# Kernel tuning notes

Hardware: AMD Instinct MI355X
Metric: run time of the kernel (lower is better)

## Reference

```python
import jax, jax.numpy as jnp
import numpy as np

N_EMBD = 1024
HEAD_SIZE = 64
B, T = 8, 2048


def setup_inputs() -> dict:
    key = jax.random.key(0)
    k1, k2, k3, k4 = jax.random.split(key, 4)
    scale = 1.0 / np.sqrt(N_EMBD)
    return {
        "x": jax.random.normal(k1, (B, T, N_EMBD), dtype=jnp.float32),
        "Wq": jax.random.normal(k2, (N_EMBD, HEAD_SIZE), dtype=jnp.float32) * scale,
        "Wk": jax.random.normal(k3, (N_EMBD, HEAD_SIZE), dtype=jnp.float32) * scale,
        "Wv": jax.random.normal(k4, (N_EMBD, HEAD_SIZE), dtype=jnp.float32) * scale,
    }


def reference(x, Wq, Wk, Wv):
    # x: [B, T, C]; projections (no bias)
    q = jnp.einsum("btc,ch->bth", x, Wq)
    k = jnp.einsum("btc,ch->bth", x, Wk)
    v = jnp.einsum("btc,ch->bth", x, Wv)
    head_size = k.shape[-1]
    # scaled scores [B, T, T]
    wei = jnp.einsum("bth,bsh->bts", q, k) * (head_size ** -0.5)
    # causal mask (lower-triangular keeps)
    Tlen = x.shape[1]
    causal = jnp.tril(jnp.ones((Tlen, Tlen), dtype=bool))
    wei = jnp.where(causal[None, :, :], wei, -jnp.inf)
    wei = jax.nn.softmax(wei, axis=-1)
    # dropout p=0 (eval) -> identity
    out = jnp.einsum("bts,bsh->bth", wei, v)
    return out
```

## Files before the change

### kernel.cpp

```cpp
#include <hip/hip_runtime.h>
#include <hip/hip_bf16.h>
#include <math.h>

#define Bn 8
#define Tn 2048
#define Cn 1024
#define Hn 64

typedef __attribute__((ext_vector_type(8))) short short8;
typedef __attribute__((ext_vector_type(4))) float floatx4;

#define ATTN_SCALE 0.18033688011112042f

__device__ inline unsigned short f2bf(float f) {
    union { float f; unsigned int u; } x; x.f = f;
    unsigned int r = x.u + 0x7fffu + ((x.u >> 16) & 1u);
    return (unsigned short)(r >> 16);
}

__device__ inline uint2 pack4bf(float4 v) {
    __hip_bfloat162 lo = __float22bfloat162_rn(make_float2(v.x, v.y));
    __hip_bfloat162 hi = __float22bfloat162_rn(make_float2(v.z, v.w));
    uint2 r;
    r.x = *reinterpret_cast<unsigned int*>(&lo);
    r.y = *reinterpret_cast<unsigned int*>(&hi);
    return r;
}

__device__ inline float rsum16(float v) {
    v += __shfl_xor(v, 1);
    v += __shfl_xor(v, 2);
    v += __shfl_xor(v, 4);
    v += __shfl_xor(v, 8);
    return v;
}

__global__ __launch_bounds__(256) void prep_w(
    const float* __restrict__ Wq, const float* __restrict__ Wk,
    const float* __restrict__ Wv, unsigned short* __restrict__ Wfrag)
{
    const int gid = blockIdx.x * 256 + threadIdx.x;
    const int c    = gid >> 11;
    const int rem  = gid & 2047;
    const int ks   = rem >> 6;
    const int lane = rem & 63;
    const int ln = lane & 15, qd = lane >> 4;
    const int mat = c >> 2, nc = c & 3;
    const float* W = (mat == 0) ? Wq : (mat == 1) ? Wk : Wv;
    const float sc = (mat == 0) ? ATTN_SCALE : 1.0f;
    const int col = nc * 16 + ln;
    unsigned short o[8];
    #pragma unroll
    for (int j = 0; j < 8; ++j)
        o[j] = f2bf(W[(size_t)(ks * 32 + qd * 8 + j) * Hn + col] * sc);
    *reinterpret_cast<short8*>(Wfrag + (size_t)gid * 8) = *reinterpret_cast<short8*>(o);
}

__global__ __launch_bounds__(256, 4) void proj_mfma(
    const float* __restrict__ x, const unsigned short* __restrict__ Wfrag,
    unsigned short* __restrict__ qbf, unsigned short* __restrict__ kfrag,
    unsigned short* __restrict__ vfrag)
{
    __shared__ unsigned short xs[2][16][136];

    const int ln   = threadIdx.x & 15;
    const int quad = (threadIdx.x >> 4) & 3;
    const int w    = threadIdx.x >> 6;
    const int lane = threadIdx.x & 63;
    const int row0 = blockIdx.x * 16;

    const int srow = threadIdx.x >> 4;
    const int sf   = threadIdx.x & 15;
    const float4* xrow4 = reinterpret_cast<const float4*>(x + (size_t)(row0 + srow) * Cn);

    floatx4 acc[3];
    #pragma unroll
    for (int i = 0; i < 3; ++i) acc[i] = (floatx4){0.f, 0.f, 0.f, 0.f};

    float4 pa_ = xrow4[sf], pb_ = xrow4[sf + 16];
    *reinterpret_cast<uint2*>(&xs[0][srow][sf * 4])      = pack4bf(pa_);
    *reinterpret_cast<uint2*>(&xs[0][srow][sf * 4 + 64]) = pack4bf(pb_);
    pa_ = xrow4[32 + sf]; pb_ = xrow4[32 + sf + 16];

    for (int c = 0; c < 8; ++c) {
        __syncthreads();
        if (c < 7) {
            *reinterpret_cast<uint2*>(&xs[(c + 1) & 1][srow][sf * 4])      = pack4bf(pa_);
            *reinterpret_cast<uint2*>(&xs[(c + 1) & 1][srow][sf * 4 + 64]) = pack4bf(pb_);
        }
        if (c < 6) {
            pa_ = xrow4[(c + 2) * 32 + sf];
            pb_ = xrow4[(c + 2) * 32 + sf + 16];
        }
        #pragma unroll
        for (int kk = 0; kk < 4; ++kk) {
            const short8 a = *reinterpret_cast<const short8*>(
                &xs[c & 1][ln][kk * 32 + quad * 8]);
            #pragma unroll
            for (int i = 0; i < 3; ++i) {
                const int cc = w * 3 + i;
                const short8 b = *reinterpret_cast<const short8*>(
                    Wfrag + ((size_t)((cc * 32) + c * 4 + kk) * 64 + lane) * 8);
                acc[i] = __builtin_amdgcn_mfma_f32_16x16x32_bf16(a, b, acc[i], 0, 0, 0);
            }
        }
    }

    const int t0   = row0 + quad * 4;
    const int b    = t0 >> 11;
    const int tloc = t0 & 2047;
    #pragma unroll
    for (int i = 0; i < 3; ++i) {
        const int idx = w * 3 + i;
        const int mat = idx >> 2, ch = idx & 3;
        if (mat == 0) {
            #pragma unroll
            for (int r = 0; r < 4; ++r)
                qbf[(size_t)(t0 + r) * Hn + ch * 16 + ln] = f2bf(acc[i][r]);
        } else if (mat == 1) {
            const int kc = tloc >> 4;
            const int ks = ch >> 1;
            const int lq = (ch & 1) * 2 + (ln >> 3);
            #pragma unroll
            for (int r = 0; r < 4; ++r) {
                const int lanep = (quad * 4 + r) + 16 * lq;
                kfrag[(((size_t)(b * 128 + kc) * 2 + ks) * 64 + lanep) * 8 + (ln & 7)]
                    = f2bf(acc[i][r]);
            }
        } else {
            const int kb32 = tloc >> 5;
            const int off  = t0 & 31;
            const int qd   = off >> 3;
            const int j0   = off & 7;
            const int lanep = ln + 16 * qd;
            ushort4 pk;
            pk.x = f2bf(acc[i][0]); pk.y = f2bf(acc[i][1]);
            pk.z = f2bf(acc[i][2]); pk.w = f2bf(acc[i][3]);
            *reinterpret_cast<ushort4*>(
                vfrag + (((size_t)(b * 64 + kb32) * 4 + ch) * 64 + lanep) * 8 + j0) = pk;
        }
    }
}

__global__ __launch_bounds__(256) void attn_mfma(
    const unsigned short* __restrict__ qbf, const unsigned short* __restrict__ kfrag,
    const unsigned short* __restrict__ vfrag, float* __restrict__ out)
{
    __shared__ unsigned short p_lds[4][2][16 * 32];
    __shared__ float o_lds[4][32][68];
    __shared__ float l_lds[4][32];

    const int j  = blockIdx.x;
    const int b  = j & 7;
    const int ti = 63 - (j >> 3);
    const int q0 = ti * 32;

    const int ln   = threadIdx.x & 15;
    const int quad = (threadIdx.x >> 4) & 3;
    const int w    = threadIdx.x >> 6;
    const int lane = threadIdx.x & 63;

    const unsigned short* qb = qbf + (size_t)b * Tn * Hn;
    const unsigned short* Kb = kfrag + (size_t)b * 131072;
    const unsigned short* Vb = vfrag + (size_t)b * 131072;

    short8 aq[2][2];
    #pragma unroll
    for (int m = 0; m < 2; ++m)
        #pragma unroll
        for (int h = 0; h < 2; ++h)
            aq[m][h] = *reinterpret_cast<const short8*>(
                qb + (size_t)(q0 + m * 16 + ln) * Hn + h * 32 + quad * 8);

    floatx4 O[2][4];
    #pragma unroll
    for (int m = 0; m < 2; ++m)
        #pragma unroll
        for (int c = 0; c < 4; ++c) O[m][c] = (floatx4){0.f, 0.f, 0.f, 0.f};
    float lp[2][4] = {{0.f,0.f,0.f,0.f},{0.f,0.f,0.f,0.f}};

    const int ntiles = (q0 >> 5) + 1;
    const int per    = (ntiles + 3) >> 2;
    const int beg    = w * per;
    const int end    = min(beg + per, ntiles);

    short8 kf[4], vf[4];
    if (beg < end) {
        #pragma unroll
        for (int u = 0; u < 4; ++u) {
            kf[u] = *reinterpret_cast<const short8*>(Kb + ((size_t)(beg * 4 + u)) * 512 + lane * 8);
            vf[u] = *reinterpret_cast<const short8*>(Vb + ((size_t)(beg * 4 + u)) * 512 + lane * 8);
        }
    }

    for (int t = beg; t < end; ++t) {
        short8 kn[4], vn[4];
        const bool more = (t + 1) < end;
        if (more) {
            #pragma unroll
            for (int u = 0; u < 4; ++u) {
                kn[u] = *reinterpret_cast<const short8*>(Kb + ((size_t)((t + 1) * 4 + u)) * 512 + lane * 8);
                vn[u] = *reinterpret_cast<const short8*>(Vb + ((size_t)((t + 1) * 4 + u)) * 512 + lane * 8);
            }
        }
        const floatx4 z = (floatx4){0.f, 0.f, 0.f, 0.f};
        floatx4 S[2][2];
        #pragma unroll
        for (int m = 0; m < 2; ++m)
            #pragma unroll
            for (int s = 0; s < 2; ++s) {
                S[m][s] = __builtin_amdgcn_mfma_f32_16x16x32_bf16(aq[m][0], kf[s * 2], z, 0, 0, 0);
                S[m][s] = __builtin_amdgcn_mfma_f32_16x16x32_bf16(aq[m][1], kf[s * 2 + 1], S[m][s], 0, 0, 0);
            }
        const bool diag = (t == ntiles - 1);
        #pragma unroll
        for (int m = 0; m < 2; ++m) {
            #pragma unroll
            for (int s = 0; s < 2; ++s) {
                #pragma unroll
                for (int r = 0; r < 4; ++r) {
                    float sv = S[m][s][r];
                    if (diag && (s * 16 + ln > m * 16 + quad * 4 + r)) sv = -1e30f;
                    const float p = exp2f(sv);
                    lp[m][r] += p;
                    p_lds[w][m][(quad * 4 + r) * 32 + s * 16 + ln] = f2bf(p);
                }
            }
        }
        __asm__ volatile("s_waitcnt lgkmcnt(0)" ::: "memory");
        short8 pa[2];
        #pragma unroll
        for (int m = 0; m < 2; ++m)
            pa[m] = *reinterpret_cast<const short8*>(&p_lds[w][m][ln * 32 + quad * 8]);
        #pragma unroll
        for (int m = 0; m < 2; ++m)
            #pragma unroll
            for (int c = 0; c < 4; ++c)
                O[m][c] = __builtin_amdgcn_mfma_f32_16x16x32_bf16(pa[m], vf[c], O[m][c], 0, 0, 0);
        #pragma unroll
        for (int u = 0; u < 4; ++u) { kf[u] = kn[u]; vf[u] = vn[u]; }
    }

    #pragma unroll
    for (int m = 0; m < 2; ++m) {
        #pragma unroll
        for (int c = 0; c < 4; ++c)
            #pragma unroll
            for (int r = 0; r < 4; ++r)
                o_lds[w][m * 16 + quad * 4 + r][c * 16 + ln] = O[m][c][r];
        #pragma unroll
        for (int r = 0; r < 4; ++r) {
            const float ls = rsum16(lp[m][r]);
            if (ln == 0) l_lds[w][m * 16 + quad * 4 + r] = ls;
        }
    }
    __syncthreads();

    const int qq  = threadIdx.x >> 3;
    const int dgp = threadIdx.x & 7;
    const float ltot = l_lds[0][qq] + l_lds[1][qq] + l_lds[2][qq] + l_lds[3][qq];
    const float inv = 1.0f / ltot;
    float* op = out + ((size_t)b * Tn + q0 + qq) * Hn + dgp * 8;
    #pragma unroll
    for (int u = 0; u < 2; ++u) {
        const float4 a0 = *reinterpret_cast<float4*>(&o_lds[0][qq][dgp * 8 + u * 4]);
        const float4 a1 = *reinterpret_cast<float4*>(&o_lds[1][qq][dgp * 8 + u * 4]);
        const float4 a2 = *reinterpret_cast<float4*>(&o_lds[2][qq][dgp * 8 + u * 4]);
        const float4 a3 = *reinterpret_cast<float4*>(&o_lds[3][qq][dgp * 8 + u * 4]);
        float4 r;
        r.x = (a0.x + a1.x + a2.x + a3.x) * inv;
        r.y = (a0.y + a1.y + a2.y + a3.y) * inv;
        r.z = (a0.z + a1.z + a2.z + a3.z) * inv;
        r.w = (a0.w + a1.w + a2.w + a3.w) * inv;
        *reinterpret_cast<float4*>(op + u * 4) = r;
    }
}

extern "C" void kernel_launch(void* const* d_in, const int* in_sizes, int n_in,
                              void* d_out, int out_size, void* d_ws, size_t ws_size,
                              hipStream_t stream) {
    (void)in_sizes; (void)n_in; (void)out_size; (void)ws_size;
    const float* x  = (const float*)d_in[0];
    const float* Wq = (const float*)d_in[1];
    const float* Wk = (const float*)d_in[2];
    const float* Wv = (const float*)d_in[3];
    float* out = (float*)d_out;

    unsigned short* Wfrag = (unsigned short*)d_ws;
    unsigned short* qbf   = Wfrag + (size_t)196608;
    unsigned short* kfr   = qbf + (size_t)Bn * Tn * Hn;
    unsigned short* vfr   = kfr + (size_t)Bn * 131072;

    prep_w<<<96, 256, 0, stream>>>(Wq, Wk, Wv, Wfrag);
    proj_mfma<<<(Bn * Tn) / 16, 256, 0, stream>>>(x, Wfrag, qbf, kfr, vfr);
    attn_mfma<<<Bn * (Tn / 32), 256, 0, stream>>>(qbf, kfr, vfr, out);
}
```

Baseline: 133.7 us.

## Halve attention query tile to 16 rows, doubling blocks and raising occupancy

The attention kernel now handles 16 query rows per block instead of 32, so the grid is twice as large. Launch bounds ask for 4 blocks per CU, and the LDS buffers shrink, with the P tile row stride padded to 40 to reduce bank conflicts. V is loaded within the current iteration instead of being prefetched a tile ahead. The bf16 conversion of P now truncates instead of rounding, and the row sum uses the same truncated value. Each K/V tile is reused by half as many queries, so global and L2 traffic roughly doubles, traded for more parallelism and better load balance over the causal triangle.

```diff
diff --git a/kernel.cpp b/kernel.cpp
--- a/kernel.cpp
+++ b/kernel.cpp
@@ -142,18 +142,18 @@
     }
 }
 
-__global__ __launch_bounds__(256) void attn_mfma(
+__global__ __launch_bounds__(256, 4) void attn_mfma(
     const unsigned short* __restrict__ qbf, const unsigned short* __restrict__ kfrag,
-    const unsigned short* __restrict__ vfrag, float* __restrict__ out)
+    const unsigned short* __restrict__ vt, float* __restrict__ out)
 {
-    __shared__ unsigned short p_lds[4][2][16 * 32];
-    __shared__ float o_lds[4][32][68];
-    __shared__ float l_lds[4][32];
+    __shared__ unsigned short p_lds[4][16 * 40];
+    __shared__ float o_lds[4][16][68];
+    __shared__ float l_lds[4][16];
 
     const int j  = blockIdx.x;
     const int b  = j & 7;
-    const int ti = 63 - (j >> 3);
-    const int q0 = ti * 32;
+    const int ti = 127 - (j >> 3);
+    const int q0 = ti * 16;
 
     const int ln   = threadIdx.x & 15;
     const int quad = (threadIdx.x >> 4) & 3;
@@ -162,118 +162,93 @@
 
     const unsigned short* qb = qbf + (size_t)b * Tn * Hn;
     const unsigned short* Kb = kfrag + (size_t)b * 131072;
-    const unsigned short* Vb = vfrag + (size_t)b * 131072;
-
-    short8 aq[2][2];
-    #pragma unroll
-    for (int m = 0; m < 2; ++m)
-        #pragma unroll
-        for (int h = 0; h < 2; ++h)
-            aq[m][h] = *reinterpret_cast<const short8*>(
-                qb + (size_t)(q0 + m * 16 + ln) * Hn + h * 32 + quad * 8);
-
-    floatx4 O[2][4];
-    #pragma unroll
-    for (int m = 0; m < 2; ++m)
-        #pragma unroll
-        for (int c = 0; c < 4; ++c) O[m][c] = (floatx4){0.f, 0.f, 0.f, 0.f};
-    float lp[2][4] = {{0.f,0.f,0.f,0.f},{0.f,0.f,0.f,0.f}};
-
-    const int ntiles = (q0 >> 5) + 1;
+    const unsigned short* Vb = vt + (size_t)b * 131072;
+
+    const short8 aq0 = *reinterpret_cast<const short8*>(qb + (size_t)(q0 + ln) * Hn + quad * 8);
+    const short8 aq1 = *reinterpret_cast<const short8*>(qb + (size_t)(q0 + ln) * Hn + 32 + quad * 8);
+
+    floatx4 O[4];
+    #pragma unroll
+    for (int c = 0; c < 4; ++c) O[c] = (floatx4){0.f, 0.f, 0.f, 0.f};
+    float lp[4] = {0.f, 0.f, 0.f, 0.f};
+
+    const int ntiles = (q0 + 47) >> 5;
     const int per    = (ntiles + 3) >> 2;
     const int beg    = w * per;
     const int end    = min(beg + per, ntiles);
-
-    short8 kf[4], vf[4];
+    unsigned short* pP = p_lds[w];
+
+    short8 kf[4];
     if (beg < end) {
         #pragma unroll
+        for (int u = 0; u < 4; ++u)
+            kf[u] = *reinterpret_cast<const short8*>(Kb + ((size_t)(beg * 4 + u)) * 512 + lane * 8);
+    }
+
+    for (int t = beg; t < end; ++t) {
+        const int tn = (t + 1 < end) ? (t + 1) : t;
+        short8 kn[4], vf[4];
+        #pragma unroll
         for (int u = 0; u < 4; ++u) {
-            kf[u] = *reinterpret_cast<const short8*>(Kb + ((size_t)(beg * 4 + u)) * 512 + lane * 8);
-            vf[u] = *reinterpret_cast<const short8*>(Vb + ((size_t)(beg * 4 + u)) * 512 + lane * 8);
-        }
-    }
-
-    for (int t = beg; t < end; ++t) {
-        short8 kn[4], vn[4];
-        const bool more = (t + 1) < end;
-        if (more) {
-            #pragma unroll
-            for (int u = 0; u < 4; ++u) {
-                kn[u] = *reinterpret_cast<const short8*>(Kb + ((size_t)((t + 1) * 4 + u)) * 512 + lane * 8);
-                vn[u] = *reinterpret_cast<const short8*>(Vb + ((size_t)((t + 1) * 4 + u)) * 512 + lane * 8);
+            kn[u] = *reinterpret_cast<const short8*>(Kb + ((size_t)(tn * 4 + u)) * 512 + lane * 8);
+            vf[u] = *reinterpret_cast<const short8*>(Vb + ((size_t)(t * 4 + u)) * 512 + lane * 8);
+        }
+
+        const floatx4 z = (floatx4){0.f, 0.f, 0.f, 0.f};
+        floatx4 S[2];
+        #pragma unroll
+        for (int s = 0; s < 2; ++s) {
+            S[s] = __builtin_amdgcn_mfma_f32_16x16x32_bf16(aq0, kf[s * 2], z, 0, 0, 0);
+            S[s] = __builtin_amdgcn_mfma_f32_16x16x32_bf16(aq1, kf[s * 2 + 1], S[s], 0, 0, 0);
+        }
+
+        const bool diag = (t == ntiles - 1);
+        #pragma unroll
+        for (int s = 0; s < 2; ++s) {
+            #pragma unroll
+            for (int r = 0; r < 4; ++r) {
+                float sv = S[s][r];
+                if (diag && (t * 32 + s * 16 + ln > q0 + quad * 4 + r)) sv = -1e30f;
+                const unsigned int pu = __float_as_uint(exp2f(sv));
+                lp[r] += __uint_as_float(pu & 0xffff0000u);
+                pP[(quad * 4 + r) * 40 + s * 16 + ln] = (unsigned short)(pu >> 16);
             }
         }
-        const floatx4 z = (floatx4){0.f, 0.f, 0.f, 0.f};
-        floatx4 S[2][2];
-        #pragma unroll
-        for (int m = 0; m < 2; ++m)
-            #pragma unroll
-            for (int s = 0; s < 2; ++s) {
-                S[m][s] = __builtin_amdgcn_mfma_f32_16x16x32_bf16(aq[m][0], kf[s * 2], z, 0, 0, 0);
-                S[m][s] = __builtin_amdgcn_mfma_f32_16x16x32_bf16(aq[m][1], kf[s * 2 + 1], S[m][s], 0, 0, 0);
-            }
-        const bool diag = (t == ntiles - 1);
-        #pragma unroll
-        for (int m = 0; m < 2; ++m) {
-            #pragma unroll
-            for (int s = 0; s < 2; ++s) {
-                #pragma unroll
-                for (int r = 0; r < 4; ++r) {
-                    float sv = S[m][s][r];
-                    if (diag && (s * 16 + ln > m * 16 + quad * 4 + r)) sv = -1e30f;
-                    const float p = exp2f(sv);
-                    lp[m][r] += p;
-                    p_lds[w][m][(quad * 4 + r) * 32 + s * 16 + ln] = f2bf(p);
-                }
-            }
-        }
         __asm__ volatile("s_waitcnt lgkmcnt(0)" ::: "memory");
-        short8 pa[2];
-        #pragma unroll
-        for (int m = 0; m < 2; ++m)
-            pa[m] = *reinterpret_cast<const short8*>(&p_lds[w][m][ln * 32 + quad * 8]);
-        #pragma unroll
-        for (int m = 0; m < 2; ++m)
-            #pragma unroll
-            for (int c = 0; c < 4; ++c)
-                O[m][c] = __builtin_amdgcn_mfma_f32_16x16x32_bf16(pa[m], vf[c], O[m][c], 0, 0, 0);
-        #pragma unroll
-        for (int u = 0; u < 4; ++u) { kf[u] = kn[u]; vf[u] = vn[u]; }
-    }
-
-    #pragma unroll
-    for (int m = 0; m < 2; ++m) {
+        const short8 pa = *reinterpret_cast<const short8*>(pP + ln * 40 + quad * 8);
         #pragma unroll
         for (int c = 0; c < 4; ++c)
-            #pragma unroll
-            for (int r = 0; r < 4; ++r)
-                o_lds[w][m * 16 + quad * 4 + r][c * 16 + ln] = O[m][c][r];
-        #pragma unroll
-        for (int r = 0; r < 4; ++r) {
-            const float ls = rsum16(lp[m][r]);
-            if (ln == 0) l_lds[w][m * 16 + quad * 4 + r] = ls;
-        }
+            O[c] = __builtin_amdgcn_mfma_f32_16x16x32_bf16(pa, vf[c], O[c], 0, 0, 0);
+        #pragma unroll
+        for (int u = 0; u < 4; ++u) kf[u] = kn[u];
+    }
+
+    #pragma unroll
+    for (int c = 0; c < 4; ++c)
+        #pragma unroll
+        for (int r = 0; r < 4; ++r)
+            o_lds[w][quad * 4 + r][c * 16 + ln] = O[c][r];
+    #pragma unroll
+    for (int r = 0; r < 4; ++r) {
+        const float ls = rsum16(lp[r]);
+        if (ln == 0) l_lds[w][quad * 4 + r] = ls;
     }
     __syncthreads();
 
-    const int qq  = threadIdx.x >> 3;
-    const int dgp = threadIdx.x & 7;
+    const int qq = threadIdx.x >> 4;
+    const int dg = threadIdx.x & 15;
     const float ltot = l_lds[0][qq] + l_lds[1][qq] + l_lds[2][qq] + l_lds[3][qq];
     const float inv = 1.0f / ltot;
-    float* op = out + ((size_t)b * Tn + q0 + qq) * Hn + dgp * 8;
-    #pragma unroll
-    for (int u = 0; u < 2; ++u) {
-        const float4 a0 = *reinterpret_cast<float4*>(&o_lds[0][qq][dgp * 8 + u * 4]);
-        const float4 a1 = *reinterpret_cast<float4*>(&o_lds[1][qq][dgp * 8 + u * 4]);
-        const float4 a2 = *reinterpret_cast<float4*>(&o_lds[2][qq][dgp * 8 + u * 4]);
-        const float4 a3 = *reinterpret_cast<float4*>(&o_lds[3][qq][dgp * 8 + u * 4]);
-        float4 r;
-        r.x = (a0.x + a1.x + a2.x + a3.x) * inv;
-        r.y = (a0.y + a1.y + a2.y + a3.y) * inv;
-        r.z = (a0.z + a1.z + a2.z + a3.z) * inv;
-        r.w = (a0.w + a1.w + a2.w + a3.w) * inv;
-        *reinterpret_cast<float4*>(op + u * 4) = r;
-    }
+    const float4 a0 = *reinterpret_cast<float4*>(&o_lds[0][qq][dg * 4]);
+    const float4 a1 = *reinterpret_cast<float4*>(&o_lds[1][qq][dg * 4]);
+    const float4 a2 = *reinterpret_cast<float4*>(&o_lds[2][qq][dg * 4]);
+    const float4 a3 = *reinterpret_cast<float4*>(&o_lds[3][qq][dg * 4]);
+    float4 r;
+    r.x = (a0.x + a1.x + a2.x + a3.x) * inv;
+    r.y = (a0.y + a1.y + a2.y + a3.y) * inv;
+    r.z = (a0.z + a1.z + a2.z + a3.z) * inv;
+    r.w = (a0.w + a1.w + a2.w + a3.w) * inv;
+    *reinterpret_cast<float4*>(out + ((size_t)b * Tn + q0 + qq) * Hn + dg * 4) = r;
 }
 
 extern "C" void kernel_launch(void* const* d_in, const int* in_sizes, int n_in,
@@ -293,5 +268,5 @@
 
     prep_w<<<96, 256, 0, stream>>>(Wq, Wk, Wv, Wfrag);
     proj_mfma<<<(Bn * Tn) / 16, 256, 0, stream>>>(x, Wfrag, qbf, kfr, vfr);
-    attn_mfma<<<Bn * (Tn / 32), 256, 0, stream>>>(qbf, kfr, vfr, out);
-}
+    attn_mfma<<<Bn * (Tn / 16), 256, 0, stream>>>(qbf, kfr, vfr, out);
+}
```

Measured after the change: 131.3 us. No clear change (-1.8%).
